# Kernel optimization log

Hardware: AMD Instinct MI355X
Metric: run time of the kernel (lower is better)

Reference implementation:

```python
import jax, jax.numpy as jnp
import numpy as np

N = 50000       # nodes
E = 800000      # edges (avg degree 16)
D_IN = 128      # input_dim
HID = 128       # hidden_dim
G_FEAT = 32     # g_feat_dim
G = 64          # number of graphs in batch
EPS = 1e-5      # BatchNorm eps


def _lin_init(key, fan_in, fan_out):
    s = 1.0 / np.sqrt(fan_in)
    return jax.random.uniform(key, (fan_in, fan_out), jnp.float32, -s, s)


def setup_inputs() -> dict:
    key = jax.random.key(0)
    ks = jax.random.split(key, 24)
    inp = {
        'x': jax.random.normal(ks[0], (N, D_IN), jnp.float32),
        'edge_index': jax.random.randint(ks[1], (2, E), 0, N, jnp.int64),
        'batch': jnp.sort(jax.random.randint(ks[2], (N,), 0, G, jnp.int64)),
        'g_feats': jax.random.normal(ks[3], (G, G_FEAT), jnp.float32),
    }
    dims = [D_IN, HID, HID]
    k = 4
    for i, din in enumerate(dims):
        inp[f'Wl{i}'] = _lin_init(ks[k], din, HID); k += 1   # lin_l (neighbors, has bias)
        inp[f'bl{i}'] = jnp.zeros((HID,), jnp.float32)
        inp[f'Wr{i}'] = _lin_init(ks[k], din, HID); k += 1   # lin_r (self, no bias in PyG)
        inp[f'gamma{i}'] = jnp.ones((HID,), jnp.float32)
        inp[f'beta{i}'] = jnp.zeros((HID,), jnp.float32)
    inp['W1'] = _lin_init(ks[k], 2 * HID + G_FEAT, HID); k += 1
    inp['b1'] = jnp.zeros((HID,), jnp.float32)
    inp['W2'] = _lin_init(ks[k], HID, HID // 2); k += 1
    inp['b2'] = jnp.zeros((HID // 2,), jnp.float32)
    inp['W3'] = _lin_init(ks[k], HID // 2, 1); k += 1
    inp['b3'] = jnp.zeros((1,), jnp.float32)
    return inp


def _sage_conv(h, src, dst, Wl, bl, Wr):
    # mean-aggregate neighbor messages x_j into target i, then lin_l(agg)+lin_r(self)
    msgs = h[src]  # [E, d] irregular gather
    agg = jax.ops.segment_sum(msgs, dst, num_segments=N)
    cnt = jax.ops.segment_sum(jnp.ones((E,), h.dtype), dst, num_segments=N)
    agg = agg / jnp.clip(cnt, 1.0)[:, None]
    return agg @ Wl + bl + h @ Wr


def _batch_norm(h, gamma, beta):
    mu = jnp.mean(h, axis=0)
    var = jnp.var(h, axis=0)
    return gamma * (h - mu) * jax.lax.rsqrt(var + EPS) + beta


def _forward(x, edge_index, batch, g_feats, convs, head):
    src, dst = edge_index[0], edge_index[1]
    h = x
    for (Wl, bl, Wr, gamma, beta) in convs:
        h = jax.nn.relu(_batch_norm(_sage_conv(h, src, dst, Wl, bl, Wr), gamma, beta))
        # dropout p=0.01: identity in eval/reference mode
    cnt = jnp.clip(jax.ops.segment_sum(jnp.ones((N,), h.dtype), batch, num_segments=G), 1.0)
    hg_mean = jax.ops.segment_sum(h, batch, num_segments=G) / cnt[:, None]
    hg_max = jax.ops.segment_max(h, batch, num_segments=G)
    W1, b1, W2, b2, W3, b3 = head
    m = jnp.concatenate([hg_mean, hg_max, g_feats], axis=1)  # [G, 2*HID+G_FEAT]
    m = jax.nn.relu(m @ W1 + b1)
    m = jax.nn.relu(m @ W2 + b2)
    return (m @ W3 + b3).reshape(-1)  # [G]


def reference(x, edge_index, batch, g_feats,
              Wl0, bl0, Wr0, gamma0, beta0,
              Wl1, bl1, Wr1, gamma1, beta1,
              Wl2, bl2, Wr2, gamma2, beta2,
              W1, b1, W2, b2, W3, b3):
    convs = [(Wl0, bl0, Wr0, gamma0, beta0),
             (Wl1, bl1, Wr1, gamma1, beta1),
             (Wl2, bl2, Wr2, gamma2, beta2)]
    head = (W1, b1, W2, b2, W3, b3)
    return _forward(x, edge_index, batch, g_feats, convs, head)
```

## Files before the change

kernel.cpp:

```cpp
#include <hip/hip_runtime.h>
#include <stdint.h>

#define NN 50000
#define NE 800000
#define HID 128
#define NG 64
#define BN_EPS 1e-5f
#define SC_NB 8
#define SC_BSZ ((NN + SC_NB - 1) / SC_NB)
#define SC_CHUNK 4096
#define SC_CHUNKS ((NE + SC_CHUNK - 1) / SC_CHUNK)
#define CAP 96
#define LAYER_BLOCKS (NN / 16)
#define NPART 64

typedef __bf16 bf16x8 __attribute__((ext_vector_type(8)));
typedef float floatx4 __attribute__((ext_vector_type(4)));

__device__ __forceinline__ float b2f(unsigned short u) {
    union { unsigned int i; float f; } x; x.i = ((unsigned int)u) << 16; return x.f;
}
__device__ __forceinline__ float blo(unsigned int d) { return __uint_as_float(d << 16); }
__device__ __forceinline__ float bhi(unsigned int d) { return __uint_as_float(d & 0xffff0000u); }
__device__ __forceinline__ unsigned short f2b(float f) {
    union { float f; unsigned int i; } x; x.f = f; unsigned int i = x.i;
    if ((i & 0x7f800000u) == 0x7f800000u) return (unsigned short)(i >> 16);
    return (unsigned short)((i + 0x7fffu + ((i >> 16) & 1u)) >> 16);
}
__device__ __forceinline__ unsigned int pack2(float f0, float f1) {
    return (((unsigned int)f2b(f1)) << 16) | f2b(f0);
}
__device__ __forceinline__ float2 bn_pair_part(const float* __restrict__ part,
                                               const float* __restrict__ gamma,
                                               const float* __restrict__ beta, int c) {
    float s = 0.f, sq = 0.f;
#pragma unroll 8
    for (int k = 0; k < NPART; ++k) {
        s += part[k * 256 + c];
        sq += part[k * 256 + 128 + c];
    }
    float mu = s * (1.f / NN);
    float var = sq * (1.f / NN) - mu * mu;
    float sc = gamma[c] * rsqrtf(var + BN_EPS);
    return make_float2(sc, beta[c] - mu * sc);
}
__device__ __forceinline__ int lbound(const int* __restrict__ batch, int val) {
    int lo = 0, hi = NN;
    while (lo < hi) { int mid = (lo + hi) >> 1; if (batch[mid] < val) lo = mid + 1; else hi = mid; }
    return lo;
}

__global__ void k_setup(const float* __restrict__ x, unsigned short* xb, int* cnt,
                        float* part, float* pool_sum, int* pool_max,
                        const float* __restrict__ Wl0, const float* __restrict__ Wr0,
                        const float* __restrict__ Wl1, const float* __restrict__ Wr1,
                        const float* __restrict__ Wl2, const float* __restrict__ Wr2,
                        unsigned short* Bp) {
    int i = blockIdx.x * 256 + threadIdx.x;
    if (i < NN * 64) {
        float2 v = ((const float2*)x)[i];
        ((unsigned int*)xb)[i] = pack2(v.x, v.y);
    }
    if (i < NN) cnt[i] = 0;
    if (i < 3 * NPART * 256) part[i] = 0.f;
    if (i < NG * HID) { pool_sum[i] = 0.f; pool_max[i] = 0; }
    if (i < 3 * 32768) {
        int layer = i >> 15;
        int r = i & 32767;
        int nt = r >> 12, kk = (r >> 9) & 7, l = (r >> 3) & 63, j = r & 7;
        int k = kk * 32 + (l >> 4) * 8 + j;
        int n = nt * 16 + (l & 15);
        const float* Wl = layer == 0 ? Wl0 : (layer == 1 ? Wl1 : Wl2);
        const float* Wr = layer == 0 ? Wr0 : (layer == 1 ? Wr1 : Wr2);
        Bp[i] = f2b((k < 128) ? Wl[k * 128 + n] : Wr[(k - 128) * 128 + n]);
    }
}

__global__ void k_scatter(const int* __restrict__ src, const int* __restrict__ dst,
                          int* cnt, int* col) {
    int bucket = blockIdx.x & (SC_NB - 1);
    int chunk = blockIdx.x / SC_NB;
    int lo = bucket * SC_BSZ, hi = lo + SC_BSZ;
    int base = chunk * SC_CHUNK;
#pragma unroll
    for (int i = 0; i < SC_CHUNK / 256; ++i) {
        int e = base + i * 256 + threadIdx.x;
        if (e < NE) {
            int d = dst[e];
            if (d >= lo && d < hi) {
                int p = atomicAdd(&cnt[d], 1);
                if (p < CAP) col[d * CAP + p] = src[e];
            }
        }
    }
}

__device__ __forceinline__ void layer_body(const unsigned short* __restrict__ h,
                                           const int* __restrict__ cnt,
                                           const int* __restrict__ col,
                                           const unsigned short* __restrict__ Bg,
                                           float* __restrict__ part,
                                           unsigned short* __restrict__ out,
                                           uint4* aggt4, uint4* selft4) {
    int t = threadIdx.x;
    int wid = t >> 6, lane = t & 63;
    const uint4* h4 = (const uint4*)h;
    {
        int slot = lane >> 4, sub = lane & 15;
        int nl = wid * 4 + slot;
        int node = blockIdx.x * 16 + nl;
        int n = cnt[node]; if (n > CAP) n = CAP;
        const int* row = col + (size_t)node * CAP;
        float a0 = 0.f, a1 = 0.f, a2 = 0.f, a3 = 0.f, a4 = 0.f, a5 = 0.f, a6 = 0.f, a7 = 0.f;
        int j = 0;
        for (; j + 4 <= n; j += 4) {
            int u0 = row[j], u1 = row[j + 1], u2 = row[j + 2], u3 = row[j + 3];
            uint4 v0 = h4[(size_t)u0 * 16 + sub];
            uint4 v1 = h4[(size_t)u1 * 16 + sub];
            uint4 v2 = h4[(size_t)u2 * 16 + sub];
            uint4 v3 = h4[(size_t)u3 * 16 + sub];
            a0 += (blo(v0.x) + blo(v1.x)) + (blo(v2.x) + blo(v3.x));
            a1 += (bhi(v0.x) + bhi(v1.x)) + (bhi(v2.x) + bhi(v3.x));
            a2 += (blo(v0.y) + blo(v1.y)) + (blo(v2.y) + blo(v3.y));
            a3 += (bhi(v0.y) + bhi(v1.y)) + (bhi(v2.y) + bhi(v3.y));
            a4 += (blo(v0.z) + blo(v1.z)) + (blo(v2.z) + blo(v3.z));
            a5 += (bhi(v0.z) + bhi(v1.z)) + (bhi(v2.z) + bhi(v3.z));
            a6 += (blo(v0.w) + blo(v1.w)) + (blo(v2.w) + blo(v3.w));
            a7 += (bhi(v0.w) + bhi(v1.w)) + (bhi(v2.w) + bhi(v3.w));
        }
        for (; j < n; ++j) {
            int u = row[j];
            uint4 v = h4[(size_t)u * 16 + sub];
            a0 += blo(v.x);  a1 += bhi(v.x);
            a2 += blo(v.y);  a3 += bhi(v.y);
            a4 += blo(v.z);  a5 += bhi(v.z);
            a6 += blo(v.w);  a7 += bhi(v.w);
        }
        float inv = (n > 0) ? 1.f / (float)n : 0.f;
        uint4 o;
        o.x = pack2(a0 * inv, a1 * inv);
        o.y = pack2(a2 * inv, a3 * inv);
        o.z = pack2(a4 * inv, a5 * inv);
        o.w = pack2(a6 * inv, a7 * inv);
        int swz = sub ^ (nl & 7);
        aggt4[nl * 16 + swz] = o;
        selft4[nl * 16 + swz] = h4[(size_t)node * 16 + sub];
    }
    __syncthreads();
    int m = lane & 15, q = lane >> 4;
    int mbase = blockIdx.x * 16;
    const bf16x8* Bv = (const bf16x8*)Bg;
    bf16x8 af[8];
#pragma unroll
    for (int kk = 0; kk < 4; ++kk) {
        int ci = (kk * 4 + q) ^ (m & 7);
        af[kk] = *(const bf16x8*)&aggt4[m * 16 + ci];
        af[4 + kk] = *(const bf16x8*)&selft4[m * 16 + ci];
    }
    floatx4 acc[2];
    acc[0] = (floatx4){0.f, 0.f, 0.f, 0.f};
    acc[1] = (floatx4){0.f, 0.f, 0.f, 0.f};
#pragma unroll
    for (int kk = 0; kk < 8; ++kk) {
#pragma unroll
        for (int ntl = 0; ntl < 2; ++ntl) {
            int nt = wid * 2 + ntl;
            bf16x8 b = Bv[(nt * 8 + kk) * 64 + lane];
            acc[ntl] = __builtin_amdgcn_mfma_f32_16x16x32_bf16(af[kk], b, acc[ntl], 0, 0, 0);
        }
    }
    float s8[2] = {0.f, 0.f}, ss8[2] = {0.f, 0.f};
#pragma unroll
    for (int ntl = 0; ntl < 2; ++ntl) {
        int c = (wid * 2 + ntl) * 16 + m;
#pragma unroll
        for (int reg = 0; reg < 4; ++reg) {
            int r = mbase + q * 4 + reg;
            float v = acc[ntl][reg];
            out[(size_t)r * 128 + c] = f2b(v);
            s8[ntl] += v;
            ss8[ntl] += v * v;
        }
        s8[ntl] += __shfl_xor(s8[ntl], 16, 64);  s8[ntl] += __shfl_xor(s8[ntl], 32, 64);
        ss8[ntl] += __shfl_xor(ss8[ntl], 16, 64); ss8[ntl] += __shfl_xor(ss8[ntl], 32, 64);
    }
    float* pb = part + (blockIdx.x & (NPART - 1)) * 256;
    if (lane < 16) {
#pragma unroll
        for (int ntl = 0; ntl < 2; ++ntl) {
            int c = (wid * 2 + ntl) * 16 + m;
            atomicAdd(&pb[c], s8[ntl]);
            atomicAdd(&pb[128 + c], ss8[ntl]);
        }
    }
}

__global__ void __launch_bounds__(256) k_layer(const unsigned short* __restrict__ h,
                                               const int* __restrict__ cnt,
                                               const int* __restrict__ col,
                                               const unsigned short* __restrict__ Bg,
                                               float* __restrict__ part,
                                               unsigned short* __restrict__ out) {
    __shared__ uint4 aggt4[256];
    __shared__ uint4 selft4[256];
    layer_body(h, cnt, col, Bg, part, out, aggt4, selft4);
}

__global__ void k_norm(const unsigned short* __restrict__ pre,
                       const float* __restrict__ part, const float* __restrict__ gamma,
                       const float* __restrict__ beta, unsigned short* __restrict__ hn) {
    __shared__ float sc[128], sh[128];
    int t = threadIdx.x;
    if (t < 128) {
        float2 p = bn_pair_part(part, gamma, beta, t);
        sc[t] = p.x; sh[t] = p.y;
    }
    __syncthreads();
#pragma unroll
    for (int ii = 0; ii < 4; ++ii) {
        int i = (blockIdx.x * 4 + ii) * 256 + t;
        if (i < NN * 16) {
            uint4 v = ((const uint4*)pre)[i];
            int cb = (i & 15) * 8;
            uint4 o;
            o.x = pack2(fmaxf(blo(v.x) * sc[cb + 0] + sh[cb + 0], 0.f),
                        fmaxf(bhi(v.x) * sc[cb + 1] + sh[cb + 1], 0.f));
            o.y = pack2(fmaxf(blo(v.y) * sc[cb + 2] + sh[cb + 2], 0.f),
                        fmaxf(bhi(v.y) * sc[cb + 3] + sh[cb + 3], 0.f));
            o.z = pack2(fmaxf(blo(v.z) * sc[cb + 4] + sh[cb + 4], 0.f),
                        fmaxf(bhi(v.z) * sc[cb + 5] + sh[cb + 5], 0.f));
            o.w = pack2(fmaxf(blo(v.w) * sc[cb + 6] + sh[cb + 6], 0.f),
                        fmaxf(bhi(v.w) * sc[cb + 7] + sh[cb + 7], 0.f));
            ((uint4*)hn)[i] = o;
        }
    }
}

__global__ void k_pool(const unsigned short* __restrict__ h, const int* __restrict__ batch,
                       const float* __restrict__ part,
                       const float* __restrict__ gamma, const float* __restrict__ beta,
                       float* pool_sum, int* pool_max) {
    int g = blockIdx.x >> 3, chunk = blockIdx.x & 7;
    int s = lbound(batch, g), e1 = lbound(batch, g + 1);
    if (s >= e1) return;
    int cnt = e1 - s;
    int per = (cnt + 7) >> 3;
    int r0 = s + chunk * per;
    int r1 = min(r0 + per, e1);
    int c = threadIdx.x & 127, half = threadIdx.x >> 7;
    float2 pr = bn_pair_part(part, gamma, beta, c);
    float sm = 0.f, mx = 0.f;
    for (int r = r0 + half; r < r1; r += 2) {
        float v = fmaxf(b2f(h[(size_t)r * 128 + c]) * pr.x + pr.y, 0.f);
        sm += v;
        mx = fmaxf(mx, v);
    }
    atomicAdd(&pool_sum[g * 128 + c], sm);
    atomicMax(&pool_max[g * 128 + c], __float_as_int(mx));
}

__global__ void __launch_bounds__(128) k_head(
    const float* __restrict__ pool_sum, const int* __restrict__ pool_max,
    const int* __restrict__ batch, const float* __restrict__ gfeats,
    const float* __restrict__ W1, const float* __restrict__ bs1,
    const float* __restrict__ W2, const float* __restrict__ bs2,
    const float* __restrict__ W3, const float* __restrict__ bs3,
    float* out) {
    __shared__ float m[288];
    __shared__ float o1[128];
    __shared__ float o2[64];
    int g = blockIdx.x, t = threadIdx.x;
    int cint = lbound(batch, g + 1) - lbound(batch, g);
    float cnt = (float)(cint < 1 ? 1 : cint);
    if (t < 128) {
        m[t] = pool_sum[g * 128 + t] / cnt;
        m[128 + t] = __int_as_float(pool_max[g * 128 + t]);
    }
    if (t < 32) m[256 + t] = gfeats[g * 32 + t];
    __syncthreads();
    float acc = bs1[t];
    for (int k = 0; k < 288; ++k) acc += m[k] * W1[k * 128 + t];
    o1[t] = fmaxf(acc, 0.f);
    __syncthreads();
    if (t < 64) {
        float a2 = bs2[t];
        for (int k = 0; k < 128; ++k) a2 += o1[k] * W2[k * 64 + t];
        o2[t] = fmaxf(a2, 0.f);
    }
    __syncthreads();
    if (t < 64) {
        float p = o2[t] * W3[t];
#pragma unroll
        for (int off = 32; off; off >>= 1) p += __shfl_down(p, off, 64);
        if (t == 0) out[g] = p + bs3[0];
    }
}

__global__ void __launch_bounds__(256) p_layer(const unsigned short* __restrict__ h,
                                               const int* __restrict__ cnt,
                                               const int* __restrict__ col,
                                               const unsigned short* __restrict__ Bg,
                                               float* __restrict__ spart,
                                               unsigned short* __restrict__ sout) {
    __shared__ uint4 aggt4[256];
    __shared__ uint4 selft4[256];
    layer_body(h, cnt, col, Bg, spart, sout, aggt4, selft4);
    __syncthreads();
    layer_body(h, cnt, col, Bg, spart, sout, aggt4, selft4);
}

extern "C" void kernel_launch(void* const* d_in, const int* in_sizes, int n_in,
                              void* d_out, int out_size, void* d_ws, size_t ws_size,
                              hipStream_t stream) {
    const float* x = (const float*)d_in[0];
    const int* ei = (const int*)d_in[1];
    const int* batch = (const int*)d_in[2];
    const float* gfeats = (const float*)d_in[3];
    const float *Wl[3], *Wr[3], *gma[3], *bta[3];
    for (int i = 0; i < 3; ++i) {
        Wl[i] = (const float*)d_in[4 + 5 * i];
        Wr[i] = (const float*)d_in[6 + 5 * i];
        gma[i] = (const float*)d_in[7 + 5 * i];
        bta[i] = (const float*)d_in[8 + 5 * i];
    }
    const float* W1 = (const float*)d_in[19];
    const float* bs1 = (const float*)d_in[20];
    const float* W2 = (const float*)d_in[21];
    const float* bs2 = (const float*)d_in[22];
    const float* W3 = (const float*)d_in[23];
    const float* bs3 = (const float*)d_in[24];

    char* p = (char*)d_ws;
    auto alloc = [&](size_t bytes) -> char* {
        char* r = p;
        p += (bytes + 255) & ~(size_t)255;
        return r;
    };
    int* cnt = (int*)alloc(NN * 4);
    int* col = (int*)alloc((size_t)NN * CAP * 4);
    float* part = (float*)alloc(3 * NPART * 256 * 4);
    float* pool_sum = (float*)alloc(NG * HID * 4);
    int* pool_max = (int*)alloc(NG * HID * 4);
    unsigned short* Bp = (unsigned short*)alloc(3 * 32768 * 2);
    unsigned short* xb = (unsigned short*)alloc((size_t)NN * 128 * 2);
    unsigned short* b0 = (unsigned short*)alloc((size_t)NN * 128 * 2);
    unsigned short* b1 = (unsigned short*)alloc((size_t)NN * 128 * 2);
    unsigned short* hn0 = (unsigned short*)alloc((size_t)NN * 128 * 2);
    float* s_part = (float*)alloc(NPART * 256 * 4);
    unsigned short* s_h = (unsigned short*)alloc((size_t)NN * 128 * 2);

    const int* srcv = ei;
    const int* dstv = ei + NE;

    k_setup<<<(NN * 64 + 255) / 256, 256, 0, stream>>>(
        x, xb, cnt, part, pool_sum, pool_max,
        Wl[0], Wr[0], Wl[1], Wr[1], Wl[2], Wr[2], Bp);
    k_scatter<<<SC_CHUNKS * SC_NB, 256, 0, stream>>>(srcv, dstv, cnt, col);

    k_layer<<<LAYER_BLOCKS, 256, 0, stream>>>(xb, cnt, col, Bp, part, b0);
    k_norm<<<(NN * 16 + 1023) / 1024, 256, 0, stream>>>(b0, part, gma[0], bta[0], hn0);
    k_layer<<<LAYER_BLOCKS, 256, 0, stream>>>(hn0, cnt, col, Bp + 32768, part + 16384, b1);
    k_norm<<<(NN * 16 + 1023) / 1024, 256, 0, stream>>>(b1, part + 16384, gma[1], bta[1], xb);
    k_layer<<<LAYER_BLOCKS, 256, 0, stream>>>(xb, cnt, col, Bp + 65536, part + 32768, b0);

    k_pool<<<NG * 8, 256, 0, stream>>>(b0, batch, part + 32768, gma[2], bta[2],
                                       pool_sum, pool_max);
    k_head<<<NG, 128, 0, stream>>>(pool_sum, pool_max, batch, gfeats,
                                   W1, bs1, W2, bs2, W3, bs3, (float*)d_out);

    p_layer<<<LAYER_BLOCKS, 256, 0, stream>>>(hn0, cnt, col, Bp + 32768, s_part, s_h);
}
```

Measured before the change: 404.7 us.

## Fuse BatchNorm+ReLU into next layer gather and drop redundant probe layer

Removes the standalone k_norm kernels. The next k_layer now computes BN scale and shift from the partial sums in its prologue and applies affine plus ReLU to every gathered neighbor row and to the self row. This saves a full write and re-read of the normalized activation buffer per layer. The trailing p_layer kernel, which redundantly recomputed a layer twice into scratch buffers, is deleted. The gather loop is also unrolled to 8 outstanding loads. The cost is extra per-neighbor FMA and max work, and rounding differs slightly because normalization now happens in fp32 before aggregation.

```diff
diff --git a/kernel.cpp b/kernel.cpp
--- a/kernel.cpp
+++ b/kernel.cpp
@@ -95,15 +95,28 @@
     }
 }
 
-__device__ __forceinline__ void layer_body(const unsigned short* __restrict__ h,
-                                           const int* __restrict__ cnt,
-                                           const int* __restrict__ col,
-                                           const unsigned short* __restrict__ Bg,
-                                           float* __restrict__ part,
-                                           unsigned short* __restrict__ out,
-                                           uint4* aggt4, uint4* selft4) {
+template <int AP>
+__global__ void __launch_bounds__(256) k_layer(const unsigned short* __restrict__ h,
+                                               const int* __restrict__ cnt,
+                                               const int* __restrict__ col,
+                                               const unsigned short* __restrict__ Bg,
+                                               const float* __restrict__ pbpart,
+                                               const float* __restrict__ pgamma,
+                                               const float* __restrict__ pbeta,
+                                               float* __restrict__ part,
+                                               unsigned short* __restrict__ out) {
+    __shared__ uint4 aggt4[256];
+    __shared__ uint4 selft4[256];
+    __shared__ float s_sc[128], s_sh[128];
     int t = threadIdx.x;
     int wid = t >> 6, lane = t & 63;
+    if (AP) {
+        if (t < 128) {
+            float2 p = bn_pair_part(pbpart, pgamma, pbeta, t);
+            s_sc[t] = p.x; s_sh[t] = p.y;
+        }
+        __syncthreads();
+    }
     const uint4* h4 = (const uint4*)h;
     {
         int slot = lane >> 4, sub = lane & 15;
@@ -111,30 +124,47 @@
         int node = blockIdx.x * 16 + nl;
         int n = cnt[node]; if (n > CAP) n = CAP;
         const int* row = col + (size_t)node * CAP;
+        float scv[8], shv[8];
+        if (AP) {
+#pragma unroll
+            for (int i = 0; i < 8; ++i) {
+                scv[i] = s_sc[sub * 8 + i];
+                shv[i] = s_sh[sub * 8 + i];
+            }
+        }
+        auto tf = [&](float f, int i) -> float {
+            return AP ? fmaxf(f * scv[i] + shv[i], 0.f) : f;
+        };
         float a0 = 0.f, a1 = 0.f, a2 = 0.f, a3 = 0.f, a4 = 0.f, a5 = 0.f, a6 = 0.f, a7 = 0.f;
+        auto acc16 = [&](uint4 v) {
+            a0 += tf(blo(v.x), 0);  a1 += tf(bhi(v.x), 1);
+            a2 += tf(blo(v.y), 2);  a3 += tf(bhi(v.y), 3);
+            a4 += tf(blo(v.z), 4);  a5 += tf(bhi(v.z), 5);
+            a6 += tf(blo(v.w), 6);  a7 += tf(bhi(v.w), 7);
+        };
         int j = 0;
+        for (; j + 8 <= n; j += 8) {
+            int us[8];
+            uint4 vs[8];
+#pragma unroll
+            for (int uu = 0; uu < 8; ++uu) us[uu] = row[j + uu];
+#pragma unroll
+            for (int uu = 0; uu < 8; ++uu) vs[uu] = h4[(size_t)us[uu] * 16 + sub];
+#pragma unroll
+            for (int uu = 0; uu < 8; ++uu) acc16(vs[uu]);
+        }
         for (; j + 4 <= n; j += 4) {
-            int u0 = row[j], u1 = row[j + 1], u2 = row[j + 2], u3 = row[j + 3];
-            uint4 v0 = h4[(size_t)u0 * 16 + sub];
-            uint4 v1 = h4[(size_t)u1 * 16 + sub];
-            uint4 v2 = h4[(size_t)u2 * 16 + sub];
-            uint4 v3 = h4[(size_t)u3 * 16 + sub];
-            a0 += (blo(v0.x) + blo(v1.x)) + (blo(v2.x) + blo(v3.x));
-            a1 += (bhi(v0.x) + bhi(v1.x)) + (bhi(v2.x) + bhi(v3.x));
-            a2 += (blo(v0.y) + blo(v1.y)) + (blo(v2.y) + blo(v3.y));
-            a3 += (bhi(v0.y) + bhi(v1.y)) + (bhi(v2.y) + bhi(v3.y));
-            a4 += (blo(v0.z) + blo(v1.z)) + (blo(v2.z) + blo(v3.z));
-            a5 += (bhi(v0.z) + bhi(v1.z)) + (bhi(v2.z) + bhi(v3.z));
-            a6 += (blo(v0.w) + blo(v1.w)) + (blo(v2.w) + blo(v3.w));
-            a7 += (bhi(v0.w) + bhi(v1.w)) + (bhi(v2.w) + bhi(v3.w));
+            int us[4];
+            uint4 vs[4];
+#pragma unroll
+            for (int uu = 0; uu < 4; ++uu) us[uu] = row[j + uu];
+#pragma unroll
+            for (int uu = 0; uu < 4; ++uu) vs[uu] = h4[(size_t)us[uu] * 16 + sub];
+#pragma unroll
+            for (int uu = 0; uu < 4; ++uu) acc16(vs[uu]);
         }
         for (; j < n; ++j) {
-            int u = row[j];
-            uint4 v = h4[(size_t)u * 16 + sub];
-            a0 += blo(v.x);  a1 += bhi(v.x);
-            a2 += blo(v.y);  a3 += bhi(v.y);
-            a4 += blo(v.z);  a5 += bhi(v.z);
-            a6 += blo(v.w);  a7 += bhi(v.w);
+            acc16(h4[(size_t)row[j] * 16 + sub]);
         }
         float inv = (n > 0) ? 1.f / (float)n : 0.f;
         uint4 o;
@@ -144,7 +174,13 @@
         o.w = pack2(a6 * inv, a7 * inv);
         int swz = sub ^ (nl & 7);
         aggt4[nl * 16 + swz] = o;
-        selft4[nl * 16 + swz] = h4[(size_t)node * 16 + sub];
+        uint4 sv = h4[(size_t)node * 16 + sub];
+        uint4 so;
+        so.x = pack2(tf(blo(sv.x), 0), tf(bhi(sv.x), 1));
+        so.y = pack2(tf(blo(sv.y), 2), tf(bhi(sv.y), 3));
+        so.z = pack2(tf(blo(sv.z), 4), tf(bhi(sv.z), 5));
+        so.w = pack2(tf(blo(sv.w), 6), tf(bhi(sv.w), 7));
+        selft4[nl * 16 + swz] = so;
     }
     __syncthreads();
     int m = lane & 15, q = lane >> 4;
@@ -191,47 +227,6 @@
             int c = (wid * 2 + ntl) * 16 + m;
             atomicAdd(&pb[c], s8[ntl]);
             atomicAdd(&pb[128 + c], ss8[ntl]);
-        }
-    }
-}
-
-__global__ void __launch_bounds__(256) k_layer(const unsigned short* __restrict__ h,
-                                               const int* __restrict__ cnt,
-                                               const int* __restrict__ col,
-                                               const unsigned short* __restrict__ Bg,
-                                               float* __restrict__ part,
-                                               unsigned short* __restrict__ out) {
-    __shared__ uint4 aggt4[256];
-    __shared__ uint4 selft4[256];
-    layer_body(h, cnt, col, Bg, part, out, aggt4, selft4);
-}
-
-__global__ void k_norm(const unsigned short* __restrict__ pre,
-                       const float* __restrict__ part, const float* __restrict__ gamma,
-                       const float* __restrict__ beta, unsigned short* __restrict__ hn) {
-    __shared__ float sc[128], sh[128];
-    int t = threadIdx.x;
-    if (t < 128) {
-        float2 p = bn_pair_part(part, gamma, beta, t);
-        sc[t] = p.x; sh[t] = p.y;
-    }
-    __syncthreads();
-#pragma unroll
-    for (int ii = 0; ii < 4; ++ii) {
-        int i = (blockIdx.x * 4 + ii) * 256 + t;
-        if (i < NN * 16) {
-            uint4 v = ((const uint4*)pre)[i];
-            int cb = (i & 15) * 8;
-            uint4 o;
-            o.x = pack2(fmaxf(blo(v.x) * sc[cb + 0] + sh[cb + 0], 0.f),
-                        fmaxf(bhi(v.x) * sc[cb + 1] + sh[cb + 1], 0.f));
-            o.y = pack2(fmaxf(blo(v.y) * sc[cb + 2] + sh[cb + 2], 0.f),
-                        fmaxf(bhi(v.y) * sc[cb + 3] + sh[cb + 3], 0.f));
-            o.z = pack2(fmaxf(blo(v.z) * sc[cb + 4] + sh[cb + 4], 0.f),
-                        fmaxf(bhi(v.z) * sc[cb + 5] + sh[cb + 5], 0.f));
-            o.w = pack2(fmaxf(blo(v.w) * sc[cb + 6] + sh[cb + 6], 0.f),
-                        fmaxf(bhi(v.w) * sc[cb + 7] + sh[cb + 7], 0.f));
-            ((uint4*)hn)[i] = o;
         }
     }
 }
@@ -296,19 +291,6 @@
     }
 }
 
-__global__ void __launch_bounds__(256) p_layer(const unsigned short* __restrict__ h,
-                                               const int* __restrict__ cnt,
-                                               const int* __restrict__ col,
-                                               const unsigned short* __restrict__ Bg,
-                                               float* __restrict__ spart,
-                                               unsigned short* __restrict__ sout) {
-    __shared__ uint4 aggt4[256];
-    __shared__ uint4 selft4[256];
-    layer_body(h, cnt, col, Bg, spart, sout, aggt4, selft4);
-    __syncthreads();
-    layer_body(h, cnt, col, Bg, spart, sout, aggt4, selft4);
-}
-
 extern "C" void kernel_launch(void* const* d_in, const int* in_sizes, int n_in,
                               void* d_out, int out_size, void* d_ws, size_t ws_size,
                               hipStream_t stream) {
@@ -345,9 +327,6 @@
     unsigned short* xb = (unsigned short*)alloc((size_t)NN * 128 * 2);
     unsigned short* b0 = (unsigned short*)alloc((size_t)NN * 128 * 2);
     unsigned short* b1 = (unsigned short*)alloc((size_t)NN * 128 * 2);
-    unsigned short* hn0 = (unsigned short*)alloc((size_t)NN * 128 * 2);
-    float* s_part = (float*)alloc(NPART * 256 * 4);
-    unsigned short* s_h = (unsigned short*)alloc((size_t)NN * 128 * 2);
 
     const int* srcv = ei;
     const int* dstv = ei + NE;
@@ -357,16 +336,15 @@
         Wl[0], Wr[0], Wl[1], Wr[1], Wl[2], Wr[2], Bp);
     k_scatter<<<SC_CHUNKS * SC_NB, 256, 0, stream>>>(srcv, dstv, cnt, col);
 
-    k_layer<<<LAYER_BLOCKS, 256, 0, stream>>>(xb, cnt, col, Bp, part, b0);
-    k_norm<<<(NN * 16 + 1023) / 1024, 256, 0, stream>>>(b0, part, gma[0], bta[0], hn0);
-    k_layer<<<LAYER_BLOCKS, 256, 0, stream>>>(hn0, cnt, col, Bp + 32768, part + 16384, b1);
-    k_norm<<<(NN * 16 + 1023) / 1024, 256, 0, stream>>>(b1, part + 16384, gma[1], bta[1], xb);
-    k_layer<<<LAYER_BLOCKS, 256, 0, stream>>>(xb, cnt, col, Bp + 65536, part + 32768, b0);
+    k_layer<0><<<LAYER_BLOCKS, 256, 0, stream>>>(xb, cnt, col, Bp,
+                                                 nullptr, nullptr, nullptr, part, b0);
+    k_layer<1><<<LAYER_BLOCKS, 256, 0, stream>>>(b0, cnt, col, Bp + 32768,
+                                                 part, gma[0], bta[0], part + 16384, b1);
+    k_layer<1><<<LAYER_BLOCKS, 256, 0, stream>>>(b1, cnt, col, Bp + 65536,
+                                                 part + 16384, gma[1], bta[1], part + 32768, b0);
 
     k_pool<<<NG * 8, 256, 0, stream>>>(b0, batch, part + 32768, gma[2], bta[2],
                                        pool_sum, pool_max);
     k_head<<<NG, 128, 0, stream>>>(pool_sum, pool_max, batch, gfeats,
                                    W1, bs1, W2, bs2, W3, bs3, (float*)d_out);
-
-    p_layer<<<LAYER_BLOCKS, 256, 0, stream>>>(hn0, cnt, col, Bp + 32768, s_part, s_h);
-}
+}
```

New measurement: 355.0 us. 1.14x faster.
